# Optimization experiments

Measured on AMD Instinct MI355X. Metric: run time of the kernel, lower is better.

The kernel has to match this reference:

```python
import jax, jax.numpy as jnp
import numpy as np

D_MODEL = 1024
N_HEADS = 16
D_K = D_MODEL // N_HEADS
SEQ = 2048
BATCH = 4


def setup_inputs() -> dict:
    key = jax.random.key(0)
    ks = jax.random.split(key, 11)
    s = 0.02
    inp = {
        'query': jax.random.normal(ks[0], (SEQ, BATCH, D_MODEL), jnp.float32),
        'key': jax.random.normal(ks[1], (SEQ, BATCH, D_MODEL), jnp.float32),
        'value': jax.random.normal(ks[2], (SEQ, BATCH, D_MODEL), jnp.float32),
        'Wq': jax.random.normal(ks[3], (D_MODEL, D_MODEL), jnp.float32) * s,
        'bq': jnp.zeros((D_MODEL,), jnp.float32),
        'Wk': jax.random.normal(ks[4], (D_MODEL, D_MODEL), jnp.float32) * s,
        'bk': jnp.zeros((D_MODEL,), jnp.float32),
        'Wv': jax.random.normal(ks[5], (D_MODEL, D_MODEL), jnp.float32) * s,
        'bv': jnp.zeros((D_MODEL,), jnp.float32),
        'Wo': jax.random.normal(ks[6], (D_MODEL, D_MODEL), jnp.float32) * s,
        'bo': jnp.zeros((D_MODEL,), jnp.float32),
    }
    return inp


def reference(query, key, value, Wq, bq, Wk, bk, Wv, bv, Wo, bo):
    # inputs are [S, B, D]; module transposes to batch-first
    q_in = jnp.swapaxes(query, 0, 1)  # [B, S, D]
    k_in = jnp.swapaxes(key, 0, 1)
    v_in = jnp.swapaxes(value, 0, 1)
    B, S, _ = q_in.shape
    # torch Linear: x @ W.T + b
    q = (q_in @ Wq.T + bq).reshape(B, S, N_HEADS, D_K)
    k = (k_in @ Wk.T + bk).reshape(B, S, N_HEADS, D_K)
    v = (v_in @ Wv.T + bv).reshape(B, S, N_HEADS, D_K)
    scale = jnp.sqrt(jnp.float32(D_K))
    scores = jnp.einsum('bqhd,bkhd->bhqk', q, k) / scale  # [B, H, S, S]
    attn = jax.nn.softmax(scores, axis=-1)
    # dropout is identity in eval / p=0
    context = jnp.einsum('bhqk,bkhd->bqhd', attn, v).reshape(B, S, D_MODEL)
    out = context @ Wo.T + bo  # [B, S, D]
    return jnp.swapaxes(out, 0, 1)  # back to [S, B, D]
```

## Files before the change

### kernel.cpp

```cpp
#include <hip/hip_runtime.h>
#include <math.h>

typedef unsigned short u16;
typedef unsigned int   u32;
typedef float f32x4  __attribute__((ext_vector_type(4)));
typedef float f32x16 __attribute__((ext_vector_type(16)));
typedef __bf16 bf16x8 __attribute__((ext_vector_type(8)));
typedef __bf16 bf16x2 __attribute__((ext_vector_type(2)));

#define SEQ   2048
#define BATCH 4
#define NH    16
#define DK    64
#define DM    1024
#define MTOT  (SEQ*BATCH)
#define SCL_QK 0.18033688011116016f

#if __has_builtin(__builtin_amdgcn_exp2f)
#define EXP2(x) __builtin_amdgcn_exp2f(x)
#else
#define EXP2(x) exp2f(x)
#endif

#define WAITCNT_VM(N) asm volatile("s_waitcnt vmcnt(" #N ")" ::: "memory")
#define BARRIER_FENCED() do {                                  \
    __builtin_amdgcn_s_barrier();                              \
    asm volatile("" ::: "memory");                             \
  } while (0)

static __device__ __forceinline__ u16 f2bf(float f) {
  __bf16 h = (__bf16)f;
  return __builtin_bit_cast(u16, h);
}
static __device__ __forceinline__ u32 pk2(float a, float b) {
  bf16x2 t = {(__bf16)a, (__bf16)b};
  return __builtin_bit_cast(u32, t);
}

typedef __attribute__((address_space(1))) const void g1_t;
typedef __attribute__((address_space(3))) void l3_t;
static __device__ __forceinline__ void gload16(const void* g, void* l) {
  __builtin_amdgcn_global_load_lds((g1_t*)g, (l3_t*)l, 16, 0, 0);
}

static __device__ __forceinline__ void cast8(const float* __restrict__ src,
                                             u16* __restrict__ dst, int i) {
  float4 a = ((const float4*)src)[2 * i];
  float4 b = ((const float4*)src)[2 * i + 1];
  uint4 r;
  r.x = pk2(a.x, a.y); r.y = pk2(a.z, a.w);
  r.z = pk2(b.x, b.y); r.w = pk2(b.z, b.w);
  ((uint4*)dst)[i] = r;
}

__global__ __launch_bounds__(256)
void cast_bf16(const float* __restrict__ src, u16* __restrict__ dst, int n8) {
  int i = blockIdx.x * 256 + threadIdx.x;
  if (i < n8) cast8(src, dst, i);
}

__global__ __launch_bounds__(256)
void cast_w(const float* __restrict__ Wq, const float* __restrict__ Wk,
            const float* __restrict__ Wv, const float* __restrict__ Wo,
            u16* __restrict__ w3, u16* __restrict__ wo_c) {
  int bid = blockIdx.x;
  int t = bid >> 9, idx = bid & 511;
  const float* src = (t == 0) ? Wq : (t == 1) ? Wk : (t == 2) ? Wv : Wo;
  u16* dst = (t < 3) ? (w3 + (size_t)t * DM * DM) : wo_c;
  cast8(src, dst, idx * 256 + threadIdx.x);
}

__global__ __launch_bounds__(256)
void cast_all(const float* __restrict__ q, const float* __restrict__ k,
              const float* __restrict__ v,
              const float* __restrict__ Wq, const float* __restrict__ Wk,
              const float* __restrict__ Wv, const float* __restrict__ Wo,
              u16* __restrict__ in_c, u16* __restrict__ w3, u16* __restrict__ wo_c) {
  int bid = blockIdx.x;
  const float* src; u16* dst; int idx;
  if (bid < 12288) {
    int t = bid >> 12; idx = bid & 4095;
    src = (t == 0) ? q : (t == 1) ? k : v;
    dst = in_c + (size_t)t * MTOT * DM;
  } else {
    int wb = bid - 12288;
    int t = wb >> 9; idx = wb & 511;
    src = (t == 0) ? Wq : (t == 1) ? Wk : (t == 2) ? Wv : Wo;
    dst = (t < 3) ? (w3 + (size_t)t * DM * DM) : wo_c;
  }
  cast8(src, dst, idx * 256 + threadIdx.x);
}

template<int OGEMM>
__global__ __launch_bounds__(256, 4)
void gemm_k(const u16* __restrict__ a0, const u16* __restrict__ a1,
            const u16* __restrict__ a2, const u16* __restrict__ w3,
            const float* __restrict__ b0, const float* __restrict__ b1,
            const float* __restrict__ b2,
            u16* __restrict__ o0, u16* __restrict__ o1, u16* __restrict__ o2,
            float* __restrict__ o3, int seg_base)
{
  constexpr int BM = 128, BN = 128, BK = 32;
  __shared__ u16 As[2][BM * BK];
  __shared__ u16 Bs[2][BN * BK];

  const int nwg = gridDim.x * gridDim.y;
  const int bid = blockIdx.y * gridDim.x + blockIdx.x;
  const int swz = (bid & 7) * (nwg >> 3) + (bid >> 3);
  const int bx  = swz % gridDim.x;
  const int by  = swz / gridDim.x;

  const int seg = OGEMM ? 0 : (seg_base + (bx >> 3));
  const int n0  = OGEMM ? bx * BN : (bx & 7) * BN;
  const int m0  = by * BM;
  const u16* A = OGEMM ? a0 : (seg == 0 ? a0 : seg == 1 ? a1 : a2);
  const u16* W = OGEMM ? w3 : (w3 + (size_t)seg * DM * DM);
  const float* bias = OGEMM ? b0 : (seg == 0 ? b0 : seg == 1 ? b1 : b2);

  const int tid  = threadIdx.x;
  const int w    = tid >> 6;
  const int lane = tid & 63;
  const int quad = lane >> 4;
  const int l15  = lane & 15;
  const int wm = (w >> 1) * 64;
  const int wn = (w & 1) * 64;

  size_t aoff[2], woff[2];
  for (int p = 0; p < 2; p++) {
    int row = w * 32 + p * 16 + (lane >> 2);
    int gm = m0 + row;
    if (OGEMM) {
      aoff[p] = (size_t)gm * DM + (lane & 3) * 8;
    } else {
      int bb = gm >> 11, s = gm & (SEQ - 1);
      aoff[p] = (size_t)(s * BATCH + bb) * DM + (lane & 3) * 8;
    }
    woff[p] = (size_t)(n0 + row) * DM + (lane & 3) * 8;
  }

  f32x4 zero4 = {0.f, 0.f, 0.f, 0.f};
  f32x4 acc[4][4];
  for (int i = 0; i < 4; i++)
    for (int j = 0; j < 4; j++)
      acc[i][j] = zero4;

  auto stage = [&](int kt, int bufi) {
#pragma unroll
    for (int p = 0; p < 2; p++) {
      gload16(A + aoff[p] + kt * BK, &As[bufi][(w * 32 + p * 16) * BK]);
      gload16(W + woff[p] + kt * BK, &Bs[bufi][(w * 32 + p * 16) * BK]);
    }
  };
  auto compute = [&](int cur) {
    bf16x8 af[4], bfr[4];
#pragma unroll
    for (int i = 0; i < 4; i++)
      af[i] = *(const bf16x8*)&As[cur][(wm + i * 16 + l15) * BK + quad * 8];
#pragma unroll
    for (int j = 0; j < 4; j++)
      bfr[j] = *(const bf16x8*)&Bs[cur][(wn + j * 16 + l15) * BK + quad * 8];
#pragma unroll
    for (int i = 0; i < 4; i++)
#pragma unroll
      for (int j = 0; j < 4; j++)
        acc[i][j] = __builtin_amdgcn_mfma_f32_16x16x32_bf16(af[i], bfr[j], acc[i][j], 0, 0, 0);
  };

  constexpr int NKT = DM / BK;
  stage(0, 0);
  int cur = 0;
  for (int kt = 0; kt < NKT - 1; kt++) {
    stage(kt + 1, cur ^ 1);
    WAITCNT_VM(4);
    BARRIER_FENCED();
    compute(cur);
    BARRIER_FENCED();
    cur ^= 1;
  }
  WAITCNT_VM(0);
  BARRIER_FENCED();
  compute(cur);

  for (int j = 0; j < 4; j++) {
    int gn = n0 + wn + j * 16 + l15;
    float bv = bias[gn];
    int h = gn >> 6, dk = gn & 63;
    for (int i = 0; i < 4; i++) {
      int gmb = m0 + wm + i * 16 + quad * 4;
      for (int r = 0; r < 4; r++) {
        int gm = gmb + r;
        float val = acc[i][j][r] + bv;
        int bb = gm >> 11, s = gm & (SEQ - 1);
        if (OGEMM) {
          o3[(size_t)(s * BATCH + bb) * DM + gn] = val;
        } else if (seg == 0) {
          o0[((size_t)(bb * NH + h) * SEQ + s) * DK + dk] = f2bf(val * SCL_QK);
        } else if (seg == 1) {
          o1[((size_t)(bb * NH + h) * SEQ + s) * DK + dk] = f2bf(val);
        } else {
          o2[((size_t)(bb * NH + h) * DK + dk) * SEQ + s] = f2bf(val);
        }
      }
    }
  }
}

__global__ __launch_bounds__(256, 4)
void attn3(const u16* __restrict__ Q, const u16* __restrict__ K,
           const u16* __restrict__ VT, u16* __restrict__ ctx)
{
  __shared__ u16 Ks[2][64 * 64];
  __shared__ u16 Vs[2][64 * 64];

  const int bh = blockIdx.x;
  const int qt = blockIdx.y;
  const int b  = bh >> 4, h = bh & 15;
  const int tid  = threadIdx.x;
  const int w    = tid >> 6;
  const int lane = tid & 63;
  const int l31  = lane & 31;
  const int hi   = lane >> 5;

  const u16* Qb = Q  + (size_t)bh * SEQ * DK;
  const u16* Kb = K  + (size_t)bh * SEQ * DK;
  const u16* Vb = VT + (size_t)bh * DK * SEQ;

  const int qbase = qt * 128 + w * 32;
  const int qrow  = qbase + l31;

  bf16x8 qf[4];
#pragma unroll
  for (int ks = 0; ks < 4; ks++)
    qf[ks] = *(const bf16x8*)&Qb[(size_t)qrow * DK + ks * 16 + hi * 8];

  const int r0 = tid >> 3;
  const int sw = (tid & 7) ^ (r0 & 7);

#define STAGE(kbb, bufi) do {                                                       \
    _Pragma("unroll")                                                               \
    for (int p = 0; p < 2; p++) {                                                   \
      int row = p * 32 + r0;                                                        \
      gload16(&Kb[(size_t)((kbb) * 64 + row) * DK + sw * 8],                        \
              &Ks[bufi][(p * 32 + w * 8) * 64]);                                    \
      gload16(&Vb[(size_t)row * SEQ + (kbb) * 64 + sw * 8],                         \
              &Vs[bufi][(p * 32 + w * 8) * 64]);                                    \
    }                                                                               \
  } while (0)

  f32x16 z16;
#pragma unroll
  for (int i = 0; i < 16; i++) z16[i] = 0.f;

  f32x16 ot0 = z16, ot1 = z16;
  float2 ls2 = {0.f, 0.f};

  u32 wp[8];

#define SOFTMAX_BLK(SA) do {                                                        \
    _Pragma("unroll")                                                               \
    for (int g = 0; g < 8; g++) {                                                   \
      float pa = EXP2(SA[2 * g]);                                                   \
      float pb = EXP2(SA[2 * g + 1]);                                               \
      ls2.x += pa; ls2.y += pb;                                                     \
      wp[g] = pk2(pa, pb);                                                          \
    }                                                                               \
  } while (0)

#define PVSTEP(VsB, KSB, KSL) do {                                                  \
    u32 a0 = wp[(KSB) * 4 + 0], a1 = wp[(KSB) * 4 + 1];                             \
    u32 a2 = wp[(KSB) * 4 + 2], a3 = wp[(KSB) * 4 + 3];                             \
    u32 s0 = hi ? a0 : a2, s1 = hi ? a1 : a3;                                       \
    u32 x0 = (u32)__shfl_xor((int)s0, 32);                                          \
    u32 x1 = (u32)__shfl_xor((int)s1, 32);                                          \
    uint4 pw;                                                                       \
    pw.x = hi ? x0 : a0; pw.y = hi ? x1 : a1;                                       \
    pw.z = hi ? a2 : x0; pw.w = hi ? a3 : x1;                                       \
    bf16x8 pf = __builtin_bit_cast(bf16x8, pw);                                     \
    const int gg = (((KSL) * 2 + hi) ^ (l31 & 7)) * 8;                              \
    bf16x8 vf0 = *(const bf16x8*)&VsB[l31 * 64 + gg];                               \
    bf16x8 vf1 = *(const bf16x8*)&VsB[(32 + l31) * 64 + gg];                        \
    ot0 = __builtin_amdgcn_mfma_f32_32x32x16_bf16(vf0, pf, ot0, 0, 0, 0);           \
    ot1 = __builtin_amdgcn_mfma_f32_32x32x16_bf16(vf1, pf, ot1, 0, 0, 0);           \
  } while (0)

#define BODY(curi) do {                                                             \
    const u16* KsB = &Ks[curi][0];                                                  \
    const u16* VsB = &Vs[curi][0];                                                  \
    f32x16 sa0 = z16, sa1 = z16;                                                    \
    _Pragma("unroll")                                                               \
    for (int ks = 0; ks < 4; ks++) {                                                \
      const int g0 = ((ks * 2 + hi) ^ (l31 & 7)) * 8;                               \
      bf16x8 kf0 = *(const bf16x8*)&KsB[l31 * 64 + g0];                             \
      bf16x8 kf1 = *(const bf16x8*)&KsB[(32 + l31) * 64 + g0];                      \
      sa0 = __builtin_amdgcn_mfma_f32_32x32x16_bf16(kf0, qf[ks], sa0, 0, 0, 0);     \
      sa1 = __builtin_amdgcn_mfma_f32_32x32x16_bf16(kf1, qf[ks], sa1, 0, 0, 0);     \
    }                                                                               \
    SOFTMAX_BLK(sa0);                                                               \
    PVSTEP(VsB, 0, 0);                                                              \
    PVSTEP(VsB, 1, 1);                                                              \
    SOFTMAX_BLK(sa1);                                                               \
    PVSTEP(VsB, 0, 2);                                                              \
    PVSTEP(VsB, 1, 3);                                                              \
  } while (0)

  constexpr int NKB = SEQ / 64;
  STAGE(0, 0);
  for (int kb = 0; kb < NKB - 1; kb++) {
    const int cur = kb & 1;
    STAGE(kb + 1, cur ^ 1);
    WAITCNT_VM(4);
    BARRIER_FENCED();
    BODY(cur);
    BARRIER_FENCED();
  }
  WAITCNT_VM(0);
  BARRIER_FENCED();
  BODY((NKB - 1) & 1);

  float ls = ls2.x + ls2.y;
  ls += __shfl_xor(ls, 32);
  float inv = 1.0f / ls;

  u16* crow = ctx + ((size_t)(b * SEQ + qrow)) * DM + h * DK;

#define STORE_BLK(OT, DKB) do {                                                     \
    _Pragma("unroll")                                                               \
    for (int t = 0; t < 4; t++) {                                                   \
      uint2 pr;                                                                     \
      pr.x = pk2(OT[4 * t + 0] * inv, OT[4 * t + 1] * inv);                         \
      pr.y = pk2(OT[4 * t + 2] * inv, OT[4 * t + 3] * inv);                         \
      *(uint2*)&crow[(DKB) * 32 + t * 8 + hi * 4] = pr;                             \
    }                                                                               \
  } while (0)

  STORE_BLK(ot0, 0);
  STORE_BLK(ot1, 1);

#undef STAGE
#undef SOFTMAX_BLK
#undef PVSTEP
#undef BODY
#undef STORE_BLK
}

extern "C" void kernel_launch(void* const* d_in, const int* in_sizes, int n_in,
                              void* d_out, int out_size, void* d_ws, size_t ws_size,
                              hipStream_t stream)
{
  const float* q  = (const float*)d_in[0];
  const float* k  = (const float*)d_in[1];
  const float* v  = (const float*)d_in[2];
  const float* Wq = (const float*)d_in[3];
  const float* bq = (const float*)d_in[4];
  const float* Wk = (const float*)d_in[5];
  const float* bk = (const float*)d_in[6];
  const float* Wv = (const float*)d_in[7];
  const float* bv = (const float*)d_in[8];
  const float* Wo = (const float*)d_in[9];
  const float* bo = (const float*)d_in[10];

  const size_t SZ_IN  = (size_t)MTOT * DM;
  const size_t SZ_W   = (size_t)DM * DM;
  const size_t NEED_FUSED = (3 * SZ_IN + 3 * SZ_W + SZ_W + 3 * SZ_IN) * 2;

  dim3 cblk(256);
  dim3 ggq(24, 64);
  dim3 ggs(8, 64);

  if (ws_size >= NEED_FUSED) {
    u16* in_c  = (u16*)d_ws;
    u16* w3    = in_c + 3 * SZ_IN;
    u16* wo_c  = w3   + 3 * SZ_W;
    u16* q_ws  = wo_c + SZ_W;
    u16* k_ws  = q_ws + SZ_IN;
    u16* vt_ws = k_ws + SZ_IN;
    u16* ctx   = in_c;

    cast_all<<<14336, cblk, 0, stream>>>(q, k, v, Wq, Wk, Wv, Wo, in_c, w3, wo_c);
    gemm_k<0><<<ggq, cblk, 0, stream>>>(in_c, in_c + SZ_IN, in_c + 2 * SZ_IN, w3,
                                        bq, bk, bv, q_ws, k_ws, vt_ws, nullptr, 0);
    attn3<<<dim3(BATCH * NH, SEQ / 128), cblk, 0, stream>>>(q_ws, k_ws, vt_ws, ctx);
    gemm_k<1><<<ggs, cblk, 0, stream>>>(ctx, ctx, ctx, wo_c,
                                        bo, bo, bo, nullptr, nullptr, nullptr,
                                        (float*)d_out, 0);
  } else {
    u16* in_c  = (u16*)d_ws;
    u16* w3    = in_c + SZ_IN;
    u16* wo_c  = w3   + 3 * SZ_W;
    u16* q_ws  = wo_c + SZ_W;
    u16* k_ws  = q_ws + SZ_IN;
    u16* vt_ws = k_ws + SZ_IN;
    u16* ctx   = in_c;

    const int NA8 = MTOT * DM / 8;
    cast_w<<<2048, cblk, 0, stream>>>(Wq, Wk, Wv, Wo, w3, wo_c);
    cast_bf16<<<NA8 / 256, cblk, 0, stream>>>(q, in_c, NA8);
    gemm_k<0><<<ggs, cblk, 0, stream>>>(in_c, in_c, in_c, w3, bq, bk, bv,
                                        q_ws, k_ws, vt_ws, nullptr, 0);
    cast_bf16<<<NA8 / 256, cblk, 0, stream>>>(k, in_c, NA8);
    gemm_k<0><<<ggs, cblk, 0, stream>>>(in_c, in_c, in_c, w3, bq, bk, bv,
                                        q_ws, k_ws, vt_ws, nullptr, 1);
    cast_bf16<<<NA8 / 256, cblk, 0, stream>>>(v, in_c, NA8);
    gemm_k<0><<<ggs, cblk, 0, stream>>>(in_c, in_c, in_c, w3, bq, bk, bv,
                                        q_ws, k_ws, vt_ws, nullptr, 2);
    attn3<<<dim3(BATCH * NH, SEQ / 128), cblk, 0, stream>>>(q_ws, k_ws, vt_ws, ctx);
    gemm_k<1><<<ggs, cblk, 0, stream>>>(ctx, ctx, ctx, wo_c,
                                        bo, bo, bo, nullptr, nullptr, nullptr,
                                        (float*)d_out, 0);
  }
}
```

Baseline: 360.7 us.

## Rework projection GEMM into 256x256 tiles with swizzled LDS and phased pipeline

The GEMM kernel now runs 512-thread blocks computing 256x256 tiles for the QKV projection and 256x128 for the output projection, with K split into 64-wide steps held in double-buffered LDS halves. Global-to-LDS loads use an XOR swizzle to avoid bank conflicts, and each K step is split into phases that interleave staging, LDS reads and MFMA bursts with explicit vmcnt waits and setprio. The aim is to raise arithmetic intensity per loaded byte and keep the matrix cores busy. In exchange it uses more registers and LDS per block, and launches fewer, larger workgroups.

```diff
diff --git a/kernel.cpp b/kernel.cpp
--- a/kernel.cpp
+++ b/kernel.cpp
@@ -24,9 +24,19 @@
 
 #define WAITCNT_VM(N) asm volatile("s_waitcnt vmcnt(" #N ")" ::: "memory")
 #define BARRIER_FENCED() do {                                  \
+    asm volatile("" ::: "memory");                             \
     __builtin_amdgcn_s_barrier();                              \
     asm volatile("" ::: "memory");                             \
   } while (0)
+
+template<int N> static __device__ __forceinline__ void vm_wait() {
+  if constexpr (N == 0)      asm volatile("s_waitcnt vmcnt(0)" ::: "memory");
+  else if constexpr (N == 3) asm volatile("s_waitcnt vmcnt(3)" ::: "memory");
+  else if constexpr (N == 4) asm volatile("s_waitcnt vmcnt(4)" ::: "memory");
+  else if constexpr (N == 6) asm volatile("s_waitcnt vmcnt(6)" ::: "memory");
+  else if constexpr (N == 8) asm volatile("s_waitcnt vmcnt(8)" ::: "memory");
+  else static_assert(N == 0, "unsupported vmcnt");
+}
 
 static __device__ __forceinline__ u16 f2bf(float f) {
   __bf16 h = (__bf16)f;
@@ -92,7 +102,7 @@
 }
 
 template<int OGEMM>
-__global__ __launch_bounds__(256, 4)
+__global__ __launch_bounds__(512, 2)
 void gemm_k(const u16* __restrict__ a0, const u16* __restrict__ a1,
             const u16* __restrict__ a2, const u16* __restrict__ w3,
             const float* __restrict__ b0, const float* __restrict__ b1,
@@ -100,9 +110,19 @@
             u16* __restrict__ o0, u16* __restrict__ o1, u16* __restrict__ o2,
             float* __restrict__ o3, int seg_base)
 {
-  constexpr int BM = 128, BN = 128, BK = 32;
-  __shared__ u16 As[2][BM * BK];
-  __shared__ u16 Bs[2][BN * BK];
+  constexpr int BN   = OGEMM ? 128 : 256;
+  constexpr int LB   = BN / 128;
+  constexpr int NREP = BN / 64;
+  constexpr int NG   = NREP / 2;
+  constexpr int VMN  = 2 + 2 * LB;
+  constexpr int VMM  = 2 + LB;
+  constexpr int VMP  = 2 * (2 + LB);
+  constexpr int WCN  = BN / 4;
+  constexpr int NKT  = DM / 64;
+  constexpr int NI   = NKT / 2;
+
+  __shared__ u16 As[2][2][256 * 32];
+  __shared__ u16 Bs[2][2][BN * 32];
 
   const int nwg = gridDim.x * gridDim.y;
   const int bid = blockIdx.y * gridDim.x + blockIdx.x;
@@ -110,86 +130,137 @@
   const int bx  = swz % gridDim.x;
   const int by  = swz / gridDim.x;
 
-  const int seg = OGEMM ? 0 : (seg_base + (bx >> 3));
-  const int n0  = OGEMM ? bx * BN : (bx & 7) * BN;
-  const int m0  = by * BM;
+  const int seg = OGEMM ? 0 : (seg_base + (bx >> 2));
+  const int n0  = OGEMM ? bx * BN : (bx & 3) * BN;
+  const int m0  = by * 256;
   const u16* A = OGEMM ? a0 : (seg == 0 ? a0 : seg == 1 ? a1 : a2);
   const u16* W = OGEMM ? w3 : (w3 + (size_t)seg * DM * DM);
   const float* bias = OGEMM ? b0 : (seg == 0 ? b0 : seg == 1 ? b1 : b2);
 
   const int tid  = threadIdx.x;
-  const int w    = tid >> 6;
+  const int wid  = tid >> 6;
   const int lane = tid & 63;
   const int quad = lane >> 4;
   const int l15  = lane & 15;
-  const int wm = (w >> 1) * 64;
-  const int wn = (w & 1) * 64;
-
-  size_t aoff[2], woff[2];
+  const int wr   = wid >> 2;
+  const int wc   = wid & 3;
+
+  const int rl = lane >> 2;
+  const int gl = (lane & 3) ^ (((lane >> 2) & 3) ^ ((lane >> 4) & 3));
+  size_t aoff[2], woff[LB];
+#pragma unroll
   for (int p = 0; p < 2; p++) {
-    int row = w * 32 + p * 16 + (lane >> 2);
-    int gm = m0 + row;
-    if (OGEMM) {
-      aoff[p] = (size_t)gm * DM + (lane & 3) * 8;
-    } else {
+    int gm = m0 + p * 128 + wid * 16 + rl;
+    if (OGEMM) aoff[p] = (size_t)gm * DM + gl * 8;
+    else {
       int bb = gm >> 11, s = gm & (SEQ - 1);
-      aoff[p] = (size_t)(s * BATCH + bb) * DM + (lane & 3) * 8;
+      aoff[p] = (size_t)(s * BATCH + bb) * DM + gl * 8;
     }
-    woff[p] = (size_t)(n0 + row) * DM + (lane & 3) * 8;
-  }
-
-  f32x4 zero4 = {0.f, 0.f, 0.f, 0.f};
-  f32x4 acc[4][4];
-  for (int i = 0; i < 4; i++)
-    for (int j = 0; j < 4; j++)
-      acc[i][j] = zero4;
-
-  auto stage = [&](int kt, int bufi) {
-#pragma unroll
-    for (int p = 0; p < 2; p++) {
-      gload16(A + aoff[p] + kt * BK, &As[bufi][(w * 32 + p * 16) * BK]);
-      gload16(W + woff[p] + kt * BK, &Bs[bufi][(w * 32 + p * 16) * BK]);
-    }
-  };
-  auto compute = [&](int cur) {
-    bf16x8 af[4], bfr[4];
-#pragma unroll
-    for (int i = 0; i < 4; i++)
-      af[i] = *(const bf16x8*)&As[cur][(wm + i * 16 + l15) * BK + quad * 8];
-#pragma unroll
-    for (int j = 0; j < 4; j++)
-      bfr[j] = *(const bf16x8*)&Bs[cur][(wn + j * 16 + l15) * BK + quad * 8];
-#pragma unroll
-    for (int i = 0; i < 4; i++)
-#pragma unroll
-      for (int j = 0; j < 4; j++)
-        acc[i][j] = __builtin_amdgcn_mfma_f32_16x16x32_bf16(af[i], bfr[j], acc[i][j], 0, 0, 0);
-  };
-
-  constexpr int NKT = DM / BK;
-  stage(0, 0);
-  int cur = 0;
-  for (int kt = 0; kt < NKT - 1; kt++) {
-    stage(kt + 1, cur ^ 1);
-    WAITCNT_VM(4);
-    BARRIER_FENCED();
-    compute(cur);
-    BARRIER_FENCED();
-    cur ^= 1;
-  }
-  WAITCNT_VM(0);
+  }
+#pragma unroll
+  for (int p = 0; p < LB; p++)
+    woff[p] = (size_t)(n0 + p * 128 + wid * 16 + rl) * DM + gl * 8;
+
+  const int sr3   = (l15 & 3) ^ ((l15 >> 2) & 3);
+  const int aro   = (quad ^ sr3) << 3;
+  const int abase = (wr * 128 + l15) * 32 + aro;
+  const int bbase = (wc * WCN + l15) * 32 + aro;
+
+  f32x4 acc[8][NREP];
+#pragma unroll
+  for (int m = 0; m < 8; m++)
+#pragma unroll
+    for (int n = 0; n < NREP; n++)
+      acc[m][n] = (f32x4){0.f, 0.f, 0.f, 0.f};
+
+  bf16x8 afr[8], bfr[NREP];
+
+#define STAGE_A(KT, KK, BUF) do {                                             \
+    _Pragma("unroll") for (int p = 0; p < 2; p++)                             \
+      gload16(A + aoff[p] + (KT) * 64 + (KK) * 32,                            \
+              &As[BUF][KK][p * 4096 + wid * 512]);                            \
+  } while (0)
+#define STAGE_B(KT, KK, BUF) do {                                             \
+    _Pragma("unroll") for (int p = 0; p < LB; p++)                            \
+      gload16(W + woff[p] + (KT) * 64 + (KK) * 32,                            \
+              &Bs[BUF][KK][p * 4096 + wid * 512]);                            \
+  } while (0)
+#define READA(BUF, KK) do {                                                   \
+    _Pragma("unroll") for (int m = 0; m < 8; m++)                             \
+      afr[m] = *(const bf16x8*)&As[BUF][KK][abase + m * 512];                 \
+  } while (0)
+#define READB(BUF, KK, NGI) do {                                              \
+    _Pragma("unroll") for (int nn = 0; nn < NG; nn++)                         \
+      bfr[(NGI) * NG + nn] =                                                  \
+        *(const bf16x8*)&Bs[BUF][KK][bbase + ((NGI) * NG + nn) * 512];        \
+  } while (0)
+#define MFMAS(NGI) do {                                                       \
+    __builtin_amdgcn_s_setprio(1);                                            \
+    _Pragma("unroll") for (int m = 0; m < 8; m++)                             \
+      _Pragma("unroll") for (int nn = 0; nn < NG; nn++)                       \
+        acc[m][(NGI) * NG + nn] = __builtin_amdgcn_mfma_f32_16x16x32_bf16(    \
+            afr[m], bfr[(NGI) * NG + nn], acc[m][(NGI) * NG + nn], 0, 0, 0);  \
+    __builtin_amdgcn_s_setprio(0);                                            \
+  } while (0)
+#define PHASE(BUF, KK, NGI, STG, VMSTMT) do {                                 \
+    if ((NGI) == 0) READA(BUF, KK);                                           \
+    READB(BUF, KK, NGI);                                                      \
+    STG;                                                                      \
+    BARRIER_FENCED();                                                         \
+    MFMAS(NGI);                                                               \
+    VMSTMT;                                                                   \
+    BARRIER_FENCED();                                                         \
+  } while (0)
+#define NOSTG ((void)0)
+#define NOVM  ((void)0)
+
+  STAGE_A(0, 0, 0); STAGE_B(0, 0, 0);
+  STAGE_A(0, 1, 0); STAGE_B(0, 1, 0);
+  STAGE_A(1, 0, 1); STAGE_B(1, 0, 1);
+  vm_wait<VMP>();
   BARRIER_FENCED();
-  compute(cur);
-
-  for (int j = 0; j < 4; j++) {
-    int gn = n0 + wn + j * 16 + l15;
+
+  for (int i = 0; i < NI - 1; i++) {
+    const int t = 2 * i;
+    PHASE(0, 0, 0, STAGE_A(t + 1, 1, 1), NOVM);
+    PHASE(0, 0, 1, STAGE_B(t + 1, 1, 1), vm_wait<VMN>());
+    PHASE(0, 1, 0, STAGE_A(t + 2, 0, 0), NOVM);
+    PHASE(0, 1, 1, STAGE_B(t + 2, 0, 0), vm_wait<VMN>());
+    PHASE(1, 0, 0, STAGE_A(t + 2, 1, 0), NOVM);
+    PHASE(1, 0, 1, STAGE_B(t + 2, 1, 0), vm_wait<VMN>());
+    PHASE(1, 1, 0, STAGE_A(t + 3, 0, 1), NOVM);
+    PHASE(1, 1, 1, STAGE_B(t + 3, 0, 1), vm_wait<VMN>());
+  }
+  PHASE(0, 0, 0, STAGE_A(NKT - 1, 1, 1), NOVM);
+  PHASE(0, 0, 1, STAGE_B(NKT - 1, 1, 1), vm_wait<VMN>());
+  PHASE(0, 1, 0, NOSTG, NOVM);
+  PHASE(0, 1, 1, NOSTG, vm_wait<VMM>());
+  PHASE(1, 0, 0, NOSTG, NOVM);
+  PHASE(1, 0, 1, NOSTG, vm_wait<0>());
+  PHASE(1, 1, 0, NOSTG, NOVM);
+  PHASE(1, 1, 1, NOSTG, NOVM);
+
+#undef STAGE_A
+#undef STAGE_B
+#undef READA
+#undef READB
+#undef MFMAS
+#undef PHASE
+#undef NOSTG
+#undef NOVM
+
+#pragma unroll
+  for (int n = 0; n < NREP; n++) {
+    int gn = n0 + wc * WCN + n * 16 + l15;
     float bv = bias[gn];
     int h = gn >> 6, dk = gn & 63;
-    for (int i = 0; i < 4; i++) {
-      int gmb = m0 + wm + i * 16 + quad * 4;
+#pragma unroll
+    for (int m = 0; m < 8; m++) {
+      int gmb = m0 + wr * 128 + m * 16 + quad * 4;
+#pragma unroll
       for (int r = 0; r < 4; r++) {
         int gm = gmb + r;
-        float val = acc[i][j][r] + bv;
+        float val = acc[m][n][r] + bv;
         int bb = gm >> 11, s = gm & (SEQ - 1);
         if (OGEMM) {
           o3[(size_t)(s * BATCH + bb) * DM + gn] = val;
@@ -364,8 +435,10 @@
   const size_t NEED_FUSED = (3 * SZ_IN + 3 * SZ_W + SZ_W + 3 * SZ_IN) * 2;
 
   dim3 cblk(256);
-  dim3 ggq(24, 64);
-  dim3 ggs(8, 64);
+  dim3 gblk(512);
+  dim3 ggq(12, 32);
+  dim3 ggq1(4, 32);
+  dim3 ggo(8, 32);
 
   if (ws_size >= NEED_FUSED) {
     u16* in_c  = (u16*)d_ws;
@@ -377,10 +450,10 @@
     u16* ctx   = in_c;
 
     cast_all<<<14336, cblk, 0, stream>>>(q, k, v, Wq, Wk, Wv, Wo, in_c, w3, wo_c);
-    gemm_k<0><<<ggq, cblk, 0, stream>>>(in_c, in_c + SZ_IN, in_c + 2 * SZ_IN, w3,
+    gemm_k<0><<<ggq, gblk, 0, stream>>>(in_c, in_c + SZ_IN, in_c + 2 * SZ_IN, w3,
                                         bq, bk, bv, q_ws, k_ws, vt_ws, nullptr, 0);
     attn3<<<dim3(BATCH * NH, SEQ / 128), cblk, 0, stream>>>(q_ws, k_ws, vt_ws, ctx);
-    gemm_k<1><<<ggs, cblk, 0, stream>>>(ctx, ctx, ctx, wo_c,
+    gemm_k<1><<<ggo, gblk, 0, stream>>>(ctx, ctx, ctx, wo_c,
                                         bo, bo, bo, nullptr, nullptr, nullptr,
                                         (float*)d_out, 0);
   } else {
@@ -395,16 +468,16 @@
     const int NA8 = MTOT * DM / 8;
     cast_w<<<2048, cblk, 0, stream>>>(Wq, Wk, Wv, Wo, w3, wo_c);
     cast_bf16<<<NA8 / 256, cblk, 0, stream>>>(q, in_c, NA8);
-    gemm_k<0><<<ggs, cblk, 0, stream>>>(in_c, in_c, in_c, w3, bq, bk, bv,
-                                        q_ws, k_ws, vt_ws, nullptr, 0);
+    gemm_k<0><<<ggq1, gblk, 0, stream>>>(in_c, in_c, in_c, w3, bq, bk, bv,
+                                         q_ws, k_ws, vt_ws, nullptr, 0);
     cast_bf16<<<NA8 / 256, cblk, 0, stream>>>(k, in_c, NA8);
-    gemm_k<0><<<ggs, cblk, 0, stream>>>(in_c, in_c, in_c, w3, bq, bk, bv,
-                                        q_ws, k_ws, vt_ws, nullptr, 1);
+    gemm_k<0><<<ggq1, gblk, 0, stream>>>(in_c, in_c, in_c, w3, bq, bk, bv,
+                                         q_ws, k_ws, vt_ws, nullptr, 1);
     cast_bf16<<<NA8 / 256, cblk, 0, stream>>>(v, in_c, NA8);
-    gemm_k<0><<<ggs, cblk, 0, stream>>>(in_c, in_c, in_c, w3, bq, bk, bv,
-                                        q_ws, k_ws, vt_ws, nullptr, 2);
+    gemm_k<0><<<ggq1, gblk, 0, stream>>>(in_c, in_c, in_c, w3, bq, bk, bv,
+                                         q_ws, k_ws, vt_ws, nullptr, 2);
     attn3<<<dim3(BATCH * NH, SEQ / 128), cblk, 0, stream>>>(q_ws, k_ws, vt_ws, ctx);
-    gemm_k<1><<<ggs, cblk, 0, stream>>>(ctx, ctx, ctx, wo_c,
+    gemm_k<1><<<ggo, gblk, 0, stream>>>(ctx, ctx, ctx, wo_c,
                                         bo, bo, bo, nullptr, nullptr, nullptr,
                                         (float*)d_out, 0);
   }
```

Result: slower. 386.6 us (+7.2%).

## Fuse fp32-to-bf16 activation cast into QKV projection GEMM A-tile loads

Applied to the files above, without the earlier changes.

The separate cast pass that wrote bf16 copies of query/key/value is removed. The QKV GEMM now loads fp32 activations into registers, packs them to bf16 and writes them to LDS, with a reworked wait/barrier schedule that overlaps these loads with the previous tile's MFMA work. This removes a full read and write of three 32 MB activation tensors plus the re-read of the bf16 copies. In exchange it doubles the A-operand global read size inside the GEMM and uses register-staged loads instead of direct global-to-LDS loads, which may raise register pressure and latency exposure.

```diff
diff --git a/kernel.cpp b/kernel.cpp
--- a/kernel.cpp
+++ b/kernel.cpp
@@ -23,10 +23,20 @@
 #endif
 
 #define WAITCNT_VM(N) asm volatile("s_waitcnt vmcnt(" #N ")" ::: "memory")
+#define WAITCNT_LGKM0() asm volatile("s_waitcnt lgkmcnt(0)" ::: "memory")
 #define BARRIER_FENCED() do {                                  \
+    asm volatile("" ::: "memory");                             \
     __builtin_amdgcn_s_barrier();                              \
     asm volatile("" ::: "memory");                             \
   } while (0)
+
+template<int N> static __device__ __forceinline__ void vm_wait() {
+  if constexpr (N == 0)      asm volatile("s_waitcnt vmcnt(0)" ::: "memory");
+  else if constexpr (N == 2) asm volatile("s_waitcnt vmcnt(2)" ::: "memory");
+  else if constexpr (N == 4) asm volatile("s_waitcnt vmcnt(4)" ::: "memory");
+  else if constexpr (N == 6) asm volatile("s_waitcnt vmcnt(6)" ::: "memory");
+  else static_assert(N == 0, "unsupported vmcnt");
+}
 
 static __device__ __forceinline__ u16 f2bf(float f) {
   __bf16 h = (__bf16)f;
@@ -70,31 +80,10 @@
   cast8(src, dst, idx * 256 + threadIdx.x);
 }
 
-__global__ __launch_bounds__(256)
-void cast_all(const float* __restrict__ q, const float* __restrict__ k,
-              const float* __restrict__ v,
-              const float* __restrict__ Wq, const float* __restrict__ Wk,
-              const float* __restrict__ Wv, const float* __restrict__ Wo,
-              u16* __restrict__ in_c, u16* __restrict__ w3, u16* __restrict__ wo_c) {
-  int bid = blockIdx.x;
-  const float* src; u16* dst; int idx;
-  if (bid < 12288) {
-    int t = bid >> 12; idx = bid & 4095;
-    src = (t == 0) ? q : (t == 1) ? k : v;
-    dst = in_c + (size_t)t * MTOT * DM;
-  } else {
-    int wb = bid - 12288;
-    int t = wb >> 9; idx = wb & 511;
-    src = (t == 0) ? Wq : (t == 1) ? Wk : (t == 2) ? Wv : Wo;
-    dst = (t < 3) ? (w3 + (size_t)t * DM * DM) : wo_c;
-  }
-  cast8(src, dst, idx * 256 + threadIdx.x);
-}
-
-template<int OGEMM>
+template<int OGEMM, int AF32>
 __global__ __launch_bounds__(256, 4)
-void gemm_k(const u16* __restrict__ a0, const u16* __restrict__ a1,
-            const u16* __restrict__ a2, const u16* __restrict__ w3,
+void gemm_k(const void* __restrict__ a0v, const void* __restrict__ a1v,
+            const void* __restrict__ a2v, const u16* __restrict__ w3,
             const float* __restrict__ b0, const float* __restrict__ b1,
             const float* __restrict__ b2,
             u16* __restrict__ o0, u16* __restrict__ o1, u16* __restrict__ o2,
@@ -110,10 +99,12 @@
   const int bx  = swz % gridDim.x;
   const int by  = swz / gridDim.x;
 
-  const int seg = OGEMM ? 0 : (seg_base + (bx >> 3));
+  const int seg = OGEMM ? 0 : (seg_base + (int)(bx >> 3));
   const int n0  = OGEMM ? bx * BN : (bx & 7) * BN;
   const int m0  = by * BM;
-  const u16* A = OGEMM ? a0 : (seg == 0 ? a0 : seg == 1 ? a1 : a2);
+  const void* Av = OGEMM ? a0v : (seg == 0 ? a0v : seg == 1 ? a1v : a2v);
+  const u16*   A16 = (const u16*)Av;
+  const float* A32 = (const float*)Av;
   const u16* W = OGEMM ? w3 : (w3 + (size_t)seg * DM * DM);
   const float* bias = OGEMM ? b0 : (seg == 0 ? b0 : seg == 1 ? b1 : b2);
 
@@ -138,18 +129,41 @@
     woff[p] = (size_t)(n0 + row) * DM + (lane & 3) * 8;
   }
 
-  f32x4 zero4 = {0.f, 0.f, 0.f, 0.f};
   f32x4 acc[4][4];
   for (int i = 0; i < 4; i++)
     for (int j = 0; j < 4; j++)
-      acc[i][j] = zero4;
-
-  auto stage = [&](int kt, int bufi) {
+      acc[i][j] = (f32x4){0.f, 0.f, 0.f, 0.f};
+
+  float4 a_nx[2][2];
+
+  auto loadA32 = [&](int kt) {
 #pragma unroll
     for (int p = 0; p < 2; p++) {
-      gload16(A + aoff[p] + kt * BK, &As[bufi][(w * 32 + p * 16) * BK]);
+      const float* s = A32 + aoff[p] + kt * BK;
+      a_nx[p][0] = *(const float4*)s;
+      a_nx[p][1] = *(const float4*)(s + 4);
+    }
+  };
+  auto writeA32 = [&](int bufi) {
+#pragma unroll
+    for (int p = 0; p < 2; p++) {
+      uint4 r;
+      r.x = pk2(a_nx[p][0].x, a_nx[p][0].y);
+      r.y = pk2(a_nx[p][0].z, a_nx[p][0].w);
+      r.z = pk2(a_nx[p][1].x, a_nx[p][1].y);
+      r.w = pk2(a_nx[p][1].z, a_nx[p][1].w);
+      *(uint4*)&As[bufi][(w * 32 + p * 16 + (lane >> 2)) * BK + (lane & 3) * 8] = r;
+    }
+  };
+  auto stageA16 = [&](int kt, int bufi) {
+#pragma unroll
+    for (int p = 0; p < 2; p++)
+      gload16(A16 + aoff[p] + kt * BK, &As[bufi][(w * 32 + p * 16) * BK]);
+  };
+  auto stageW = [&](int kt, int bufi) {
+#pragma unroll
+    for (int p = 0; p < 2; p++)
       gload16(W + woff[p] + kt * BK, &Bs[bufi][(w * 32 + p * 16) * BK]);
-    }
   };
   auto compute = [&](int cur) {
     bf16x8 af[4], bfr[4];
@@ -167,19 +181,43 @@
   };
 
   constexpr int NKT = DM / BK;
-  stage(0, 0);
-  int cur = 0;
-  for (int kt = 0; kt < NKT - 1; kt++) {
-    stage(kt + 1, cur ^ 1);
-    WAITCNT_VM(4);
+  if constexpr (AF32) {
+    loadA32(0);
+    stageW(0, 0);
+    vm_wait<2>();
+    writeA32(0);
+    WAITCNT_LGKM0();
+    for (int kt = 0; kt < NKT - 1; kt++) {
+      const int cur = kt & 1;
+      loadA32(kt + 1);
+      stageW(kt + 1, cur ^ 1);
+      vm_wait<6>();
+      BARRIER_FENCED();
+      compute(cur);
+      vm_wait<2>();
+      writeA32(cur ^ 1);
+      WAITCNT_LGKM0();
+      BARRIER_FENCED();
+    }
+    vm_wait<0>();
     BARRIER_FENCED();
-    compute(cur);
+    compute((NKT - 1) & 1);
+  } else {
+    stageA16(0, 0);
+    stageW(0, 0);
+    for (int kt = 0; kt < NKT - 1; kt++) {
+      const int cur = kt & 1;
+      stageA16(kt + 1, cur ^ 1);
+      stageW(kt + 1, cur ^ 1);
+      vm_wait<4>();
+      BARRIER_FENCED();
+      compute(cur);
+      BARRIER_FENCED();
+    }
+    vm_wait<0>();
     BARRIER_FENCED();
-    cur ^= 1;
+    compute((NKT - 1) & 1);
   }
-  WAITCNT_VM(0);
-  BARRIER_FENCED();
-  compute(cur);
 
   for (int j = 0; j < 4; j++) {
     int gn = n0 + wn + j * 16 + l15;
@@ -361,28 +399,29 @@
 
   const size_t SZ_IN  = (size_t)MTOT * DM;
   const size_t SZ_W   = (size_t)DM * DM;
-  const size_t NEED_FUSED = (3 * SZ_IN + 3 * SZ_W + SZ_W + 3 * SZ_IN) * 2;
+  const size_t NEED_FUSED = (4 * SZ_W + 4 * SZ_IN) * 2;
 
   dim3 cblk(256);
   dim3 ggq(24, 64);
   dim3 ggs(8, 64);
+  dim3 agrid(BATCH * NH, SEQ / 128);
 
   if (ws_size >= NEED_FUSED) {
-    u16* in_c  = (u16*)d_ws;
-    u16* w3    = in_c + 3 * SZ_IN;
-    u16* wo_c  = w3   + 3 * SZ_W;
-    u16* q_ws  = wo_c + SZ_W;
-    u16* k_ws  = q_ws + SZ_IN;
-    u16* vt_ws = k_ws + SZ_IN;
-    u16* ctx   = in_c;
-
-    cast_all<<<14336, cblk, 0, stream>>>(q, k, v, Wq, Wk, Wv, Wo, in_c, w3, wo_c);
-    gemm_k<0><<<ggq, cblk, 0, stream>>>(in_c, in_c + SZ_IN, in_c + 2 * SZ_IN, w3,
-                                        bq, bk, bv, q_ws, k_ws, vt_ws, nullptr, 0);
-    attn3<<<dim3(BATCH * NH, SEQ / 128), cblk, 0, stream>>>(q_ws, k_ws, vt_ws, ctx);
-    gemm_k<1><<<ggs, cblk, 0, stream>>>(ctx, ctx, ctx, wo_c,
-                                        bo, bo, bo, nullptr, nullptr, nullptr,
-                                        (float*)d_out, 0);
+    u16* w3    = (u16*)d_ws;
+    u16* wo_c  = w3    + 3 * SZ_W;
+    u16* q_ws  = wo_c  + SZ_W;
+    u16* k_ws  = q_ws  + SZ_IN;
+    u16* vt_ws = k_ws  + SZ_IN;
+    u16* ctx   = vt_ws + SZ_IN;
+
+    cast_w<<<2048, cblk, 0, stream>>>(Wq, Wk, Wv, Wo, w3, wo_c);
+    gemm_k<0, 1><<<ggq, cblk, 0, stream>>>(q, k, v, w3,
+                                           bq, bk, bv, q_ws, k_ws, vt_ws,
+                                           nullptr, 0);
+    attn3<<<agrid, cblk, 0, stream>>>(q_ws, k_ws, vt_ws, ctx);
+    gemm_k<1, 0><<<ggs, cblk, 0, stream>>>(ctx, ctx, ctx, wo_c,
+                                           bo, bo, bo, nullptr, nullptr, nullptr,
+                                           (float*)d_out, 0);
   } else {
     u16* in_c  = (u16*)d_ws;
     u16* w3    = in_c + SZ_IN;
@@ -395,17 +434,17 @@
     const int NA8 = MTOT * DM / 8;
     cast_w<<<2048, cblk, 0, stream>>>(Wq, Wk, Wv, Wo, w3, wo_c);
     cast_bf16<<<NA8 / 256, cblk, 0, stream>>>(q, in_c, NA8);
-    gemm_k<0><<<ggs, cblk, 0, stream>>>(in_c, in_c, in_c, w3, bq, bk, bv,
-                                        q_ws, k_ws, vt_ws, nullptr, 0);
+    gemm_k<0, 0><<<ggs, cblk, 0, stream>>>(in_c, in_c, in_c, w3, bq, bk, bv,
+                                           q_ws, k_ws, vt_ws, nullptr, 0);
     cast_bf16<<<NA8 / 256, cblk, 0, stream>>>(k, in_c, NA8);
-    gemm_k<0><<<ggs, cblk, 0, stream>>>(in_c, in_c, in_c, w3, bq, bk, bv,
-                                        q_ws, k_ws, vt_ws, nullptr, 1);
+    gemm_k<0, 0><<<ggs, cblk, 0, stream>>>(in_c, in_c, in_c, w3, bq, bk, bv,
+                                           q_ws, k_ws, vt_ws, nullptr, 1);
     cast_bf16<<<NA8 / 256, cblk, 0, stream>>>(v, in_c, NA8);
-    gemm_k<0><<<ggs, cblk, 0, stream>>>(in_c, in_c, in_c, w3, bq, bk, bv,
-                                        q_ws, k_ws, vt_ws, nullptr, 2);
-    attn3<<<dim3(BATCH * NH, SEQ / 128), cblk, 0, stream>>>(q_ws, k_ws, vt_ws, ctx);
-    gemm_k<1><<<ggs, cblk, 0, stream>>>(ctx, ctx, ctx, wo_c,
-                                        bo, bo, bo, nullptr, nullptr, nullptr,
-                                        (float*)d_out, 0);
+    gemm_k<0, 0><<<ggs, cblk, 0, stream>>>(in_c, in_c, in_c, w3, bq, bk, bv,
+                                           q_ws, k_ws, vt_ws, nullptr, 2);
+    attn3<<<agrid, cblk, 0, stream>>>(q_ws, k_ws, vt_ws, ctx);
+    gemm_k<1, 0><<<ggs, cblk, 0, stream>>>(ctx, ctx, ctx, wo_c,
+                                           bo, bo, bo, nullptr, nullptr, nullptr,
+                                           (float*)d_out, 0);
   }
 }
```

After: 370.4 us. 2.7% more time.
